# Kernel optimization log

Measured on AMD Instinct MI355X. Metric: run time of the kernel, lower is better.

The kernel has to match this reference:

```python
import jax, jax.numpy as jnp
import numpy as np

N_NODES = 100000
N_INCID = 2000000
N_HEDGES = 300000
IN_DIM = 92
H_DIM = 64
ATTR_DIM = 35
HOUT_DIM = 128
N_GRAPHS = 512
N_LAYERS = 3
MSG_DIM = 2 * H_DIM + ATTR_DIM  # 163, matches Linear(2*node_fea_dim+hedge_fea_dim, out_dim)


def _segment_mean(vals, ids, num_segments):
    s = jax.ops.segment_sum(vals, ids, num_segments=num_segments)
    c = jax.ops.segment_sum(jnp.ones((vals.shape[0],), vals.dtype), ids, num_segments=num_segments)
    return s / jnp.maximum(c, 1.0)[:, None]


def setup_inputs() -> dict:
    key = jax.random.key(0)
    ks = jax.random.split(key, 16)
    x = jax.random.normal(ks[0], (N_NODES, IN_DIM), jnp.float32)
    incid_nodes = jax.random.randint(ks[1], (N_INCID,), 0, N_NODES)
    incid_hedges = jax.random.randint(ks[2], (N_INCID,), 0, N_HEDGES)
    hedge_attr = jax.random.normal(ks[3], (N_HEDGES, ATTR_DIM), jnp.float32)
    batch = jnp.sort(jax.random.randint(ks[4], (N_NODES,), 0, N_GRAPHS))
    def lin(k, fi, fo):
        lim = 1.0 / np.sqrt(fi)
        kw, kb = jax.random.split(k)
        return (jax.random.uniform(kw, (fi, fo), jnp.float32, -lim, lim),
                jax.random.uniform(kb, (fo,), jnp.float32, -lim, lim))
    W_embed, b_embed = lin(ks[5], IN_DIM, H_DIM)
    Wf, bf = [], []
    Wc, bc = [], []
    for l in range(N_LAYERS):
        w, b = lin(jax.random.fold_in(ks[6], l), MSG_DIM, H_DIM)
        Wf.append(w); bf.append(b)
        w, b = lin(jax.random.fold_in(ks[7], l), MSG_DIM, H_DIM)
        Wc.append(w); bc.append(b)
    Wf = jnp.stack(Wf); bf = jnp.stack(bf)
    Wc = jnp.stack(Wc); bc = jnp.stack(bc)
    W_proj, b_proj = lin(ks[8], H_DIM, HOUT_DIM)
    W_out, b_out = lin(ks[9], HOUT_DIM, 1)
    return {"x": x, "incid_nodes": incid_nodes, "incid_hedges": incid_hedges,
            "hedge_attr": hedge_attr, "batch": batch,
            "W_embed": W_embed, "b_embed": b_embed,
            "Wf": Wf, "bf": bf, "Wc": Wc, "bc": bc,
            "W_proj": W_proj, "b_proj": b_proj, "W_out": W_out, "b_out": b_out}


def reference(x, incid_nodes, incid_hedges, hedge_attr, batch,
              W_embed, b_embed, Wf, bf, Wc, bc, W_proj, b_proj, W_out, b_out):
    h = x @ W_embed + b_embed  # [N, H_DIM] embed
    node_cnt = jax.ops.segment_sum(jnp.ones((N_INCID,), h.dtype), incid_nodes,
                                   num_segments=N_NODES)
    has_incid = (node_cnt > 0)[:, None]
    # mean of hedge_attr over hedges containing each node (constant across layers)
    node_a = _segment_mean(hedge_attr[incid_hedges], incid_nodes, N_NODES)
    for l in range(N_LAYERS):
        # per-hedge mean of member node features (the normalized node_hedge_adj @ x)
        hedge_mean = _segment_mean(h[incid_nodes], incid_hedges, N_HEDGES)  # [H, H_DIM]
        # per-node mean over incident hedges of the message components
        node_h = _segment_mean(hedge_mean[incid_hedges], incid_nodes, N_NODES)
        x_part = jnp.where(has_incid, h, 0.0)  # mean over incidences of constant x_i
        z = jnp.concatenate([x_part, node_h, node_a], axis=1)  # [N, MSG_DIM]
        z_f = z @ Wf[l] + bf[l]
        z_c = z @ Wc[l] + bc[l]
        h = jax.nn.softplus(jax.nn.sigmoid(z_f) * jax.nn.softplus(z_c) + h)
    pooled = _segment_mean(h, batch, N_GRAPHS)  # scatter-mean global pooling
    p = jax.nn.softplus(pooled @ W_proj + b_proj)
    return p @ W_out + b_out  # [N_GRAPHS, 1]
```

## Files before the change

### kernel.cpp

```cpp
#include <hip/hip_runtime.h>
#include <hip/hip_bf16.h>

#define N_NODES 100000
#define N_INCID 2000000
#define N_HEDGES 300000
#define IN_DIM 92
#define H_DIM 64
#define ATTR_DIM 35
#define ATTR_PAIRS 18
#define HOUT_DIM 128
#define N_GRAPHS 512
#define N_LAYERS 3
#define MSG_DIM 163
#define KPAIRS 96
#define ZLDS 100
#define EPAIRS 48
#define ELDS 50

#define IPB 8192
#define NBLK 245
#define ESHIFT 9
#define NB_E 586
#define NSHIFT 8
#define NB_N 391

typedef short bf16x8 __attribute__((ext_vector_type(8)));
typedef float f32x4 __attribute__((ext_vector_type(4)));

__device__ __forceinline__ float softplusf(float x) {
    return fmaxf(x, 0.f) + __logf(1.f + __expf(-fabsf(x)));
}
__device__ __forceinline__ float sigmoidf(float x) {
    return __builtin_amdgcn_rcpf(1.f + __expf(-x));
}
__device__ __forceinline__ float2 bf2_to_f2(unsigned v) {
    union { unsigned u; float f; } a, b;
    a.u = v << 16;
    b.u = v & 0xffff0000u;
    return make_float2(a.f, b.f);
}
__device__ __forceinline__ unsigned f2_to_bf2(float x, float y) {
    union { float f; unsigned u; } a, b;
    a.f = x; b.f = y;
    unsigned lo = (a.u + 0x7fffu + ((a.u >> 16) & 1u)) >> 16;
    unsigned hi = ((b.u + 0x7fffu + ((b.u >> 16) & 1u)) >> 16) << 16;
    return lo | hi;
}

__global__ void embpack_k(const float* __restrict__ W, unsigned* __restrict__ BtE) {
    int idx = blockIdx.x * 256 + threadIdx.x;
    if (idx >= 64 * EPAIRS) return;
    int c = idx / EPAIRS, p = idx - c * EPAIRS;
    int k0 = 2 * p, k1 = 2 * p + 1;
    float v0 = (k0 < IN_DIM) ? W[k0 * 64 + c] : 0.f;
    float v1 = (k1 < IN_DIM) ? W[k1 * 64 + c] : 0.f;
    BtE[idx] = f2_to_bf2(v0, v1);
}

__global__ void __launch_bounds__(256)
embed_mfma_k(const float* __restrict__ x, const unsigned* __restrict__ BtE,
             const float* __restrict__ be, const int* __restrict__ ncnt,
             float* __restrict__ h, unsigned* __restrict__ hb,
             unsigned* __restrict__ zb) {
    __shared__ unsigned zsu[64][ELDS];
    __shared__ unsigned btu[64][ELDS];
    int node0 = blockIdx.x * 64;
    int t = threadIdx.x;
    for (int idx = t; idx < 64 * EPAIRS; idx += 256) {
        int r = idx / EPAIRS, p = idx - r * EPAIRS;
        int node = node0 + r;
        unsigned pr = 0u;
        if (node < N_NODES && p < 46) {
            float2 f = *(const float2*)(x + (size_t)node * IN_DIM + 2 * p);
            pr = f2_to_bf2(f.x, f.y);
        }
        zsu[r][p] = pr;
    }
    for (int idx = t; idx < 64 * EPAIRS; idx += 256) {
        int c = idx / EPAIRS, p = idx - c * EPAIRS;
        btu[c][p] = BtE[idx];
    }
    __syncthreads();
    int w = t >> 6, lane = t & 63, row16 = lane & 15, kg = lane >> 4;
    f32x4 acc[4];
#pragma unroll
    for (int n = 0; n < 4; ++n) acc[n] = (f32x4){0.f, 0.f, 0.f, 0.f};
#pragma unroll
    for (int ks = 0; ks < 3; ++ks) {
        int pbase = ks * 16 + kg * 4;
        bf16x8 a = *(const bf16x8*)&zsu[w * 16 + row16][pbase];
#pragma unroll
        for (int n = 0; n < 4; ++n) {
            bf16x8 b = *(const bf16x8*)&btu[n * 16 + row16][pbase];
            acc[n] = __builtin_amdgcn_mfma_f32_16x16x32_bf16(a, b, acc[n], 0, 0, 0);
        }
    }
#pragma unroll
    for (int i = 0; i < 4; ++i) {
        int node = node0 + w * 16 + kg * 4 + i;
        if (node < N_NODES) {
            bool has = ncnt[node] > 0;
#pragma unroll
            for (int n = 0; n < 4; ++n) {
                int d = n * 16 + row16;
                float nv = acc[n][i] + be[d];
                h[node * 64 + d] = nv;
                float other = __shfl_xor(nv, 1);
                if ((d & 1) == 0) {
                    unsigned pr = f2_to_bf2(nv, other);
                    hb[node * 32 + (d >> 1)] = pr;
                    zb[(size_t)node * KPAIRS + (d >> 1)] = has ? pr : 0u;
                }
            }
        }
    }
}

__global__ void attrconv_k(const float* __restrict__ hattr, unsigned* __restrict__ hab) {
    int idx = blockIdx.x * 256 + threadIdx.x;
    if (idx >= N_HEDGES * ATTR_PAIRS) return;
    int e = idx / ATTR_PAIRS, p = idx - e * ATTR_PAIRS;
    int d0 = 2 * p, d1 = 2 * p + 1;
    float v0 = hattr[e * ATTR_DIM + d0];
    float v1 = (d1 < ATTR_DIM) ? hattr[e * ATTR_DIM + d1] : 0.f;
    hab[idx] = f2_to_bf2(v0, v1);
}

__global__ void btpack_k(const float* __restrict__ Wf, const float* __restrict__ Wc,
                         unsigned* __restrict__ Btb) {
    int idx = blockIdx.x * 256 + threadIdx.x;
    if (idx >= N_LAYERS * 128 * KPAIRS) return;
    int l = idx / (128 * KPAIRS);
    int rem = idx - l * 128 * KPAIRS;
    int c = rem / KPAIRS, p = rem - c * KPAIRS;
    int k0 = 2 * p, k1 = 2 * p + 1;
    const float* W = (c < 64) ? (Wf + (size_t)l * MSG_DIM * 64) : (Wc + (size_t)l * MSG_DIM * 64);
    int cc = c & 63;
    float v0 = (k0 < MSG_DIM) ? W[k0 * 64 + cc] : 0.f;
    float v1 = (k1 < MSG_DIM) ? W[k1 * 64 + cc] : 0.f;
    Btb[idx] = f2_to_bf2(v0, v1);
}

__global__ void sorthist_k(const int* __restrict__ key, int* __restrict__ hist,
                           int kshift, int NB) {
    __shared__ int cnt[640];
    int blk = blockIdx.x;
    for (int i = threadIdx.x; i < NB; i += 256) cnt[i] = 0;
    __syncthreads();
    int base = blk * IPB;
    int end = min(base + IPB, N_INCID);
    for (int i = base + threadIdx.x; i < end; i += 256)
        atomicAdd(&cnt[key[i] >> kshift], 1);
    __syncthreads();
    for (int i = threadIdx.x; i < NB; i += 256) hist[blk * NB + i] = cnt[i];
}

__global__ void scanR1_k(const int* __restrict__ in, int* __restrict__ out,
                         int* __restrict__ bsum, int n, int NB) {
    __shared__ int tmp[256];
    int gid = blockIdx.x * 256 + threadIdx.x;
    int v = 0;
    if (gid < n) {
        int bucket = gid / NBLK, blk = gid - bucket * NBLK;
        v = in[blk * NB + bucket];
    }
    tmp[threadIdx.x] = v;
    __syncthreads();
    for (int o = 1; o < 256; o <<= 1) {
        int t = (threadIdx.x >= o) ? tmp[threadIdx.x - o] : 0;
        __syncthreads();
        tmp[threadIdx.x] += t;
        __syncthreads();
    }
    if (gid < n) out[gid] = tmp[threadIdx.x] - v;
    if (threadIdx.x == 255) bsum[blockIdx.x] = tmp[255];
}

__global__ void scan2_k(int* __restrict__ bsum, int nb) {
    __shared__ int tmp[256];
    __shared__ int carry;
    if (threadIdx.x == 0) carry = 0;
    __syncthreads();
    for (int base = 0; base < nb; base += 256) {
        int gid = base + threadIdx.x;
        int v = (gid < nb) ? bsum[gid] : 0;
        tmp[threadIdx.x] = v;
        __syncthreads();
        for (int o = 1; o < 256; o <<= 1) {
            int t = (threadIdx.x >= o) ? tmp[threadIdx.x - o] : 0;
            __syncthreads();
            tmp[threadIdx.x] += t;
            __syncthreads();
        }
        if (gid < nb) bsum[gid] = tmp[threadIdx.x] - v + carry;
        __syncthreads();
        if (threadIdx.x == 0) carry += tmp[255];
        __syncthreads();
    }
}

__global__ void scan3_k(int* __restrict__ out, const int* __restrict__ bsum, int n) {
    int gid = blockIdx.x * 256 + threadIdx.x;
    if (gid < n) out[gid] += bsum[blockIdx.x];
}

__global__ void sortscat_k(const int* __restrict__ key, const int* __restrict__ val,
                           const int* __restrict__ soff, uint2* __restrict__ stage,
                           int kshift, int NB) {
    __shared__ int cur[640], bas[640];
    int blk = blockIdx.x;
    for (int i = threadIdx.x; i < NB; i += 256) {
        cur[i] = 0;
        bas[i] = soff[i * NBLK + blk];
    }
    __syncthreads();
    int base = blk * IPB;
    int end = min(base + IPB, N_INCID);
    for (int i = base + threadIdx.x; i < end; i += 256) {
        int k = key[i], b = k >> kshift;
        int d = bas[b] + atomicAdd(&cur[b], 1);
        stage[d] = make_uint2((unsigned)k, (unsigned)val[i]);
    }
}

__global__ void sortfine_k(const uint2* __restrict__ stage, const int* __restrict__ soff,
                           int* __restrict__ csr, int* __restrict__ koff,
                           float* __restrict__ krcp, int* __restrict__ kcnt,
                           int kshift, int NB, int NKEYS, int nlog) {
    __shared__ int cnt[512], off[512], cur[512];
    int b = blockIdx.x;
    int KPB = 1 << kshift;
    int kbase = b << kshift;
    int base = soff[b * NBLK];
    int end = (b == NB - 1) ? N_INCID : soff[(b + 1) * NBLK];
    for (int i = threadIdx.x; i < KPB; i += 256) cnt[i] = 0;
    __syncthreads();
    for (int i = base + threadIdx.x; i < end; i += 256)
        atomicAdd(&cnt[(int)stage[i].x - kbase], 1);
    __syncthreads();
    if (threadIdx.x == 0) {
        int run = 0;
        for (int k = 0; k < KPB; ++k) { off[k] = run; run += cnt[k]; }
    }
    __syncthreads();
    for (int k = threadIdx.x; k < KPB; k += 256) {
        int gk = kbase + k;
        if (gk < NKEYS) {
            koff[gk] = base + off[k];
            krcp[gk] = 1.0f / (float)max(cnt[k], 1);
            kcnt[gk] = cnt[k];
        }
        cur[k] = 0;
    }
    __syncthreads();
    for (int i = base + threadIdx.x; i < end; i += 256) {
        uint2 it = stage[i];
        int lk = (int)it.x - kbase;
        int pos = base + off[lk] + atomicAdd(&cur[lk], 1);
        csr[pos] = (int)it.y;
    }
}

__global__ void sentinel_k(int* __restrict__ eoff, int* __restrict__ noff) {
    if (threadIdx.x == 0) eoff[N_HEDGES] = N_INCID;
    if (threadIdx.x == 1) noff[N_NODES] = N_INCID;
}

__global__ void hmean_k(const int* __restrict__ eoff, const int* __restrict__ csr_en,
                        const uint2* __restrict__ hbv, const float* __restrict__ ercp,
                        uint2* __restrict__ hmv) {
    int idx = blockIdx.x * 256 + threadIdx.x;
    int e = idx >> 5, l = idx & 31;
    if (e >= N_HEDGES) return;
    int sub = l >> 4, q = l & 15;
    int s = eoff[e], t = eoff[e + 1];
    float a0 = 0.f, a1 = 0.f, a2 = 0.f, a3 = 0.f;
    for (int base = s; base < t; base += 32) {
        int cnt = min(32, t - base);
        int myidx = (base + l < t) ? csr_en[base + l] : 0;
        for (int j = 0; j < cnt; j += 16) {
            uint2 v[8];
#pragma unroll
            for (int w = 0; w < 8; ++w) {
                int mem = j + 2 * w + sub;
                int nq = __shfl(myidx, mem, 32);
                v[w] = (mem < cnt) ? hbv[nq * 16 + q] : make_uint2(0u, 0u);
            }
#pragma unroll
            for (int w = 0; w < 8; ++w) {
                float2 f0 = bf2_to_f2(v[w].x), f1 = bf2_to_f2(v[w].y);
                a0 += f0.x; a1 += f0.y; a2 += f1.x; a3 += f1.y;
            }
        }
    }
    a0 += __shfl_xor(a0, 16);
    a1 += __shfl_xor(a1, 16);
    a2 += __shfl_xor(a2, 16);
    a3 += __shfl_xor(a3, 16);
    if (sub == 0) {
        float rc = ercp[e];
        hmv[e * 16 + q] = make_uint2(f2_to_bf2(a0 * rc, a1 * rc), f2_to_bf2(a2 * rc, a3 * rc));
    }
}

__global__ void nodeh_k(const int* __restrict__ noff, const int* __restrict__ csr_ne,
                        const uint2* __restrict__ hmv, const float* __restrict__ nrcp,
                        uint2* __restrict__ zbv) {
    int idx = blockIdx.x * 256 + threadIdx.x;
    int n = idx >> 5, l = idx & 31;
    if (n >= N_NODES) return;
    int sub = l >> 4, q = l & 15;
    int s = noff[n], t = noff[n + 1];
    float a0 = 0.f, a1 = 0.f, a2 = 0.f, a3 = 0.f;
    for (int base = s; base < t; base += 32) {
        int cnt = min(32, t - base);
        int myidx = (base + l < t) ? csr_ne[base + l] : 0;
        for (int j = 0; j < cnt; j += 16) {
            uint2 v[8];
#pragma unroll
            for (int w = 0; w < 8; ++w) {
                int mem = j + 2 * w + sub;
                int eq = __shfl(myidx, mem, 32);
                v[w] = (mem < cnt) ? hmv[eq * 16 + q] : make_uint2(0u, 0u);
            }
#pragma unroll
            for (int w = 0; w < 8; ++w) {
                float2 f0 = bf2_to_f2(v[w].x), f1 = bf2_to_f2(v[w].y);
                a0 += f0.x; a1 += f0.y; a2 += f1.x; a3 += f1.y;
            }
        }
    }
    a0 += __shfl_xor(a0, 16);
    a1 += __shfl_xor(a1, 16);
    a2 += __shfl_xor(a2, 16);
    a3 += __shfl_xor(a3, 16);
    if (sub == 0) {
        float rc = nrcp[n];
        zbv[(size_t)n * (KPAIRS / 2) + 16 + q] =
            make_uint2(f2_to_bf2(a0 * rc, a1 * rc), f2_to_bf2(a2 * rc, a3 * rc));
    }
}

__global__ void nodea_k(const int* __restrict__ noff, const int* __restrict__ csr_ne,
                        const uint2* __restrict__ habv, const float* __restrict__ nrcp,
                        uint2* __restrict__ zbv) {
    int idx = blockIdx.x * 256 + threadIdx.x;
    int n = idx >> 5, l = idx & 31;
    if (n >= N_NODES) return;
    int sub = l >> 4, q = l & 15;
    bool act = (q < ATTR_PAIRS / 2);
    int s = noff[n], t = noff[n + 1];
    float a0 = 0.f, a1 = 0.f, a2 = 0.f, a3 = 0.f;
    for (int base = s; base < t; base += 32) {
        int cnt = min(32, t - base);
        int myidx = (base + l < t) ? csr_ne[base + l] : 0;
        for (int j = 0; j < cnt; j += 16) {
            uint2 v[8];
#pragma unroll
            for (int w = 0; w < 8; ++w) {
                int mem = j + 2 * w + sub;
                int eq = __shfl(myidx, mem, 32);
                v[w] = (act && mem < cnt) ? habv[eq * (ATTR_PAIRS / 2) + q] : make_uint2(0u, 0u);
            }
#pragma unroll
            for (int w = 0; w < 8; ++w) {
                float2 f0 = bf2_to_f2(v[w].x), f1 = bf2_to_f2(v[w].y);
                a0 += f0.x; a1 += f0.y; a2 += f1.x; a3 += f1.y;
            }
        }
    }
    a0 += __shfl_xor(a0, 16);
    a1 += __shfl_xor(a1, 16);
    a2 += __shfl_xor(a2, 16);
    a3 += __shfl_xor(a3, 16);
    if (sub == 0) {
        float rc = nrcp[n];
        uint2 pr = act ? make_uint2(f2_to_bf2(a0 * rc, a1 * rc), f2_to_bf2(a2 * rc, a3 * rc))
                       : make_uint2(0u, 0u);
        zbv[(size_t)n * (KPAIRS / 2) + 32 + q] = pr;
    }
}

__global__ void __launch_bounds__(256)
layer_mfma_k(const unsigned* __restrict__ Btl, const float* __restrict__ bfv,
             const float* __restrict__ bcv, const int* __restrict__ ncnt,
             unsigned* __restrict__ zb, float* __restrict__ h,
             unsigned* __restrict__ hb) {
    __shared__ unsigned zsu[64][ZLDS];
    int node0 = blockIdx.x * 64;
    int t = threadIdx.x;
    int w = t >> 6, lane = t & 63;
    int row16 = lane & 15, kg = lane >> 4;

    uint4 bregF[6], bregC[6];
    {
        const uint4* bv = (const uint4*)Btl;
        int colF = w * 16 + row16;
        int colC = colF + 64;
#pragma unroll
        for (int ks = 0; ks < 6; ++ks) {
            bregF[ks] = bv[colF * 24 + ks * 4 + kg];
            bregC[ks] = bv[colC * 24 + ks * 4 + kg];
        }
    }
    {
        const uint4* zv = (const uint4*)zb;
        for (int idx = t; idx < 64 * 24; idx += 256) {
            int r = idx / 24, p4 = idx - r * 24;
            int node = node0 + r;
            uint4 v = make_uint4(0u, 0u, 0u, 0u);
            if (node < N_NODES) v = zv[(size_t)node * 24 + p4];
            *(uint4*)&zsu[r][p4 * 4] = v;
        }
    }
    __syncthreads();

    f32x4 accF[4], accC[4];
#pragma unroll
    for (int n = 0; n < 4; ++n) {
        accF[n] = (f32x4){0.f, 0.f, 0.f, 0.f};
        accC[n] = (f32x4){0.f, 0.f, 0.f, 0.f};
    }

#pragma unroll
    for (int ks = 0; ks < 6; ++ks) {
        int pbase = ks * 16 + kg * 4;
        bf16x8 bF = *(const bf16x8*)&bregF[ks];
        bf16x8 bC = *(const bf16x8*)&bregC[ks];
#pragma unroll
        for (int rb = 0; rb < 4; ++rb) {
            bf16x8 a = *(const bf16x8*)&zsu[rb * 16 + row16][pbase];
            accF[rb] = __builtin_amdgcn_mfma_f32_16x16x32_bf16(a, bF, accF[rb], 0, 0, 0);
            accC[rb] = __builtin_amdgcn_mfma_f32_16x16x32_bf16(a, bC, accC[rb], 0, 0, 0);
        }
    }

    int d = w * 16 + row16;
    float bfd = bfv[d], bcd = bcv[d];
#pragma unroll
    for (int rb = 0; rb < 4; ++rb) {
#pragma unroll
        for (int i = 0; i < 4; ++i) {
            int node = node0 + rb * 16 + kg * 4 + i;
            if (node < N_NODES) {
                bool has = ncnt[node] > 0;
                float f = accF[rb][i] + bfd;
                float c = accC[rb][i] + bcd;
                float hv = h[node * 64 + d];
                float nv = softplusf(sigmoidf(f) * softplusf(c) + hv);
                h[node * 64 + d] = nv;
                float other = __shfl_xor(nv, 1);
                if ((d & 1) == 0) {
                    unsigned pr = f2_to_bf2(nv, other);
                    hb[node * 32 + (d >> 1)] = pr;
                    zb[(size_t)node * KPAIRS + (d >> 1)] = has ? pr : 0u;
                }
            }
        }
    }
}

__global__ void gstart_k(const int* __restrict__ batch, int* __restrict__ gstart) {
    int g = blockIdx.x * 256 + threadIdx.x;
    if (g > N_GRAPHS) return;
    int lo = 0, hi = N_NODES;
    while (lo < hi) {
        int mid = (lo + hi) >> 1;
        if (batch[mid] < g) lo = mid + 1; else hi = mid;
    }
    gstart[g] = lo;
}

__global__ void poolhead_k(const float* __restrict__ h, const int* __restrict__ gstart,
                           const float* __restrict__ Wp, const float* __restrict__ bp,
                           const float* __restrict__ Wo, const float* __restrict__ bo,
                           float* __restrict__ out) {
    __shared__ float partial[4][64];
    __shared__ float pm[64];
    __shared__ float pr[128];
    int g = blockIdx.x, t = threadIdx.x;
    int s = gstart[g], e = gstart[g + 1];
    int w = t >> 6, lane = t & 63;
    float acc = 0.f;
    for (int n = s + w; n < e; n += 4) acc += h[n * 64 + lane];
    partial[w][lane] = acc;
    __syncthreads();
    if (t < 64) {
        float c = fmaxf((float)(e - s), 1.0f);
        pm[t] = (partial[0][t] + partial[1][t] + partial[2][t] + partial[3][t]) / c;
    }
    __syncthreads();
    if (t < 128) {
        float a = bp[t];
#pragma unroll 4
        for (int k = 0; k < 64; ++k) a += pm[k] * Wp[k * HOUT_DIM + t];
        pr[t] = softplusf(a) * Wo[t];
    }
    __syncthreads();
    if (t < 64) {
        float v = pr[t] + pr[t + 64];
        for (int o = 32; o > 0; o >>= 1) v += __shfl_down(v, o);
        if (t == 0) out[g] = v + bo[0];
    }
}

extern "C" void kernel_launch(void* const* d_in, const int* in_sizes, int n_in,
                              void* d_out, int out_size, void* d_ws, size_t ws_size,
                              hipStream_t stream) {
    const float* x       = (const float*)d_in[0];
    const int*   inc_n   = (const int*)d_in[1];
    const int*   inc_e   = (const int*)d_in[2];
    const float* hattr   = (const float*)d_in[3];
    const int*   batch   = (const int*)d_in[4];
    const float* W_embed = (const float*)d_in[5];
    const float* b_embed = (const float*)d_in[6];
    const float* Wf      = (const float*)d_in[7];
    const float* bf      = (const float*)d_in[8];
    const float* Wc      = (const float*)d_in[9];
    const float* bc      = (const float*)d_in[10];
    const float* W_proj  = (const float*)d_in[11];
    const float* b_proj  = (const float*)d_in[12];
    const float* W_out   = (const float*)d_in[13];
    const float* b_out   = (const float*)d_in[14];
    float* out = (float*)d_out;

    char* ws = (char*)d_ws;
    size_t off = 0;
    auto alloc = [&](size_t bytes) {
        void* p = ws + off;
        off = (off + bytes + 255) & ~(size_t)255;
        return p;
    };
    float*    h      = (float*)alloc((size_t)N_NODES * 64 * 4);
    unsigned* hb     = (unsigned*)alloc((size_t)N_NODES * 32 * 4);
    unsigned* hmean  = (unsigned*)alloc((size_t)N_HEDGES * 32 * 4);
    unsigned* zb     = (unsigned*)alloc((size_t)N_NODES * KPAIRS * 4);
    unsigned* hab    = (unsigned*)alloc((size_t)N_HEDGES * ATTR_PAIRS * 4);
    unsigned* Btb    = (unsigned*)alloc((size_t)N_LAYERS * 128 * KPAIRS * 4);
    unsigned* BtE    = (unsigned*)alloc((size_t)64 * EPAIRS * 4);
    int*      ncnt   = (int*)alloc((size_t)N_NODES * 4);
    int*      ecnt   = (int*)alloc((size_t)N_HEDGES * 4);
    float*    nrcp   = (float*)alloc((size_t)N_NODES * 4);
    float*    ercp   = (float*)alloc((size_t)N_HEDGES * 4);
    int*      eoff   = (int*)alloc((size_t)(N_HEDGES + 1) * 4);
    int*      noff   = (int*)alloc((size_t)(N_NODES + 1) * 4);
    int*      csr_en = (int*)alloc((size_t)N_INCID * 4);
    int*      csr_ne = (int*)alloc((size_t)N_INCID * 4);
    int*      hist   = (int*)alloc((size_t)NB_E * NBLK * 4);
    int*      soff   = (int*)alloc((size_t)NB_E * NBLK * 4);
    int*      bsum   = (int*)alloc((size_t)2048 * 4);
    int*      gstart = (int*)alloc((size_t)(N_GRAPHS + 1) * 4);
    uint2*    stage  = (uint2*)hmean;

    {
        int nlog = NB_E * NBLK;
        int nsb = (nlog + 255) / 256;
        sorthist_k<<<NBLK, 256, 0, stream>>>(inc_e, hist, ESHIFT, NB_E);
        scanR1_k<<<nsb, 256, 0, stream>>>(hist, soff, bsum, nlog, NB_E);
        scan2_k<<<1, 256, 0, stream>>>(bsum, nsb);
        scan3_k<<<nsb, 256, 0, stream>>>(soff, bsum, nlog);
        sortscat_k<<<NBLK, 256, 0, stream>>>(inc_e, inc_n, soff, stage, ESHIFT, NB_E);
        sortfine_k<<<NB_E, 256, 0, stream>>>(stage, soff, csr_en, eoff, ercp, ecnt,
                                             ESHIFT, NB_E, N_HEDGES, nlog);
    }
    {
        int nlog = NB_N * NBLK;
        int nsb = (nlog + 255) / 256;
        sorthist_k<<<NBLK, 256, 0, stream>>>(inc_n, hist, NSHIFT, NB_N);
        scanR1_k<<<nsb, 256, 0, stream>>>(hist, soff, bsum, nlog, NB_N);
        scan2_k<<<1, 256, 0, stream>>>(bsum, nsb);
        scan3_k<<<nsb, 256, 0, stream>>>(soff, bsum, nlog);
        sortscat_k<<<NBLK, 256, 0, stream>>>(inc_n, inc_e, soff, stage, NSHIFT, NB_N);
        sortfine_k<<<NB_N, 256, 0, stream>>>(stage, soff, csr_ne, noff, nrcp, ncnt,
                                             NSHIFT, NB_N, N_NODES, nlog);
    }
    sentinel_k<<<1, 64, 0, stream>>>(eoff, noff);

    embpack_k<<<(64 * EPAIRS + 255) / 256, 256, 0, stream>>>(W_embed, BtE);
    embed_mfma_k<<<(N_NODES + 63) / 64, 256, 0, stream>>>(x, BtE, b_embed, ncnt, h, hb, zb);
    attrconv_k<<<(N_HEDGES * ATTR_PAIRS + 255) / 256, 256, 0, stream>>>(hattr, hab);
    btpack_k<<<(N_LAYERS * 128 * KPAIRS + 255) / 256, 256, 0, stream>>>(Wf, Wc, Btb);
    nodea_k<<<(N_NODES * 32) / 256, 256, 0, stream>>>(noff, csr_ne, (const uint2*)hab, nrcp,
                                                      (uint2*)zb);

    for (int l = 0; l < N_LAYERS; ++l) {
        hmean_k<<<(N_HEDGES * 32) / 256, 256, 0, stream>>>(eoff, csr_en, (const uint2*)hb, ercp,
                                                           (uint2*)hmean);
        nodeh_k<<<(N_NODES * 32) / 256, 256, 0, stream>>>(noff, csr_ne, (const uint2*)hmean, nrcp,
                                                          (uint2*)zb);
        layer_mfma_k<<<(N_NODES + 63) / 64, 256, 0, stream>>>(Btb + (size_t)l * 128 * KPAIRS,
                                                              bf + l * 64, bc + l * 64,
                                                              ncnt, zb, h, hb);
    }
    gstart_k<<<(N_GRAPHS + 1 + 255) / 256, 256, 0, stream>>>(batch, gstart);
    poolhead_k<<<N_GRAPHS, 256, 0, stream>>>(h, gstart, W_proj, b_proj, W_out, b_out, out);
}
```

Measured before the change: 639.2 us.

## Pack sort staging into 32-bit words, parallelize fine-sort scan, use packed f32x2 accumulation

```diff
diff --git a/kernel.cpp b/kernel.cpp
--- a/kernel.cpp
+++ b/kernel.cpp
@@ -23,9 +23,11 @@
 #define NB_E 586
 #define NSHIFT 8
 #define NB_N 391
+#define VALBITS 21
 
 typedef short bf16x8 __attribute__((ext_vector_type(8)));
 typedef float f32x4 __attribute__((ext_vector_type(4)));
+typedef float f32x2 __attribute__((ext_vector_type(2)));
 
 __device__ __forceinline__ float softplusf(float x) {
     return fmaxf(x, 0.f) + __logf(1.f + __expf(-fabsf(x)));
@@ -33,11 +35,11 @@
 __device__ __forceinline__ float sigmoidf(float x) {
     return __builtin_amdgcn_rcpf(1.f + __expf(-x));
 }
+__device__ __forceinline__ float u2f(unsigned u) {
+    union { unsigned u; float f; } x; x.u = u; return x.f;
+}
 __device__ __forceinline__ float2 bf2_to_f2(unsigned v) {
-    union { unsigned u; float f; } a, b;
-    a.u = v << 16;
-    b.u = v & 0xffff0000u;
-    return make_float2(a.f, b.f);
+    return make_float2(u2f(v << 16), u2f(v & 0xffff0000u));
 }
 __device__ __forceinline__ unsigned f2_to_bf2(float x, float y) {
     union { float f; unsigned u; } a, b;
@@ -205,7 +207,7 @@
 }
 
 __global__ void sortscat_k(const int* __restrict__ key, const int* __restrict__ val,
-                           const int* __restrict__ soff, uint2* __restrict__ stage,
+                           const int* __restrict__ soff, unsigned* __restrict__ stage,
                            int kshift, int NB) {
     __shared__ int cur[640], bas[640];
     int blk = blockIdx.x;
@@ -216,34 +218,48 @@
     __syncthreads();
     int base = blk * IPB;
     int end = min(base + IPB, N_INCID);
+    unsigned kmaskbits = (1u << kshift) - 1u;
     for (int i = base + threadIdx.x; i < end; i += 256) {
         int k = key[i], b = k >> kshift;
         int d = bas[b] + atomicAdd(&cur[b], 1);
-        stage[d] = make_uint2((unsigned)k, (unsigned)val[i]);
-    }
-}
-
-__global__ void sortfine_k(const uint2* __restrict__ stage, const int* __restrict__ soff,
+        stage[d] = (((unsigned)k & kmaskbits) << VALBITS) | (unsigned)val[i];
+    }
+}
+
+__global__ void sortfine_k(const unsigned* __restrict__ stage, const int* __restrict__ soff,
                            int* __restrict__ csr, int* __restrict__ koff,
                            float* __restrict__ krcp, int* __restrict__ kcnt,
-                           int kshift, int NB, int NKEYS, int nlog) {
+                           int kshift, int NB, int NKEYS) {
     __shared__ int cnt[512], off[512], cur[512];
+    __shared__ int ts[256];
     int b = blockIdx.x;
+    int tid = threadIdx.x;
     int KPB = 1 << kshift;
     int kbase = b << kshift;
     int base = soff[b * NBLK];
     int end = (b == NB - 1) ? N_INCID : soff[(b + 1) * NBLK];
-    for (int i = threadIdx.x; i < KPB; i += 256) cnt[i] = 0;
-    __syncthreads();
-    for (int i = base + threadIdx.x; i < end; i += 256)
-        atomicAdd(&cnt[(int)stage[i].x - kbase], 1);
-    __syncthreads();
-    if (threadIdx.x == 0) {
-        int run = 0;
-        for (int k = 0; k < KPB; ++k) { off[k] = run; run += cnt[k]; }
-    }
-    __syncthreads();
-    for (int k = threadIdx.x; k < KPB; k += 256) {
+    for (int i = tid; i < KPB; i += 256) cnt[i] = 0;
+    __syncthreads();
+    for (int i = base + tid; i < end; i += 256)
+        atomicAdd(&cnt[stage[i] >> VALBITS], 1);
+    __syncthreads();
+    int half = KPB >> 1;
+    int c0 = 0, c1 = 0;
+    if (tid < half) { c0 = cnt[2 * tid]; c1 = cnt[2 * tid + 1]; ts[tid] = c0 + c1; }
+    __syncthreads();
+    for (int o = 1; o < 256; o <<= 1) {
+        int v = (tid >= o && tid < half) ? ts[tid - o] : 0;
+        __syncthreads();
+        if (tid < half) ts[tid] += v;
+        __syncthreads();
+    }
+    if (tid < half) {
+        int ex = ts[tid] - (c0 + c1);
+        off[2 * tid] = ex;
+        off[2 * tid + 1] = ex + c0;
+    }
+    __syncthreads();
+    for (int k = tid; k < KPB; k += 256) {
         int gk = kbase + k;
         if (gk < NKEYS) {
             koff[gk] = base + off[k];
@@ -253,11 +269,11 @@
         cur[k] = 0;
     }
     __syncthreads();
-    for (int i = base + threadIdx.x; i < end; i += 256) {
-        uint2 it = stage[i];
-        int lk = (int)it.x - kbase;
+    for (int i = base + tid; i < end; i += 256) {
+        unsigned it = stage[i];
+        int lk = (int)(it >> VALBITS);
         int pos = base + off[lk] + atomicAdd(&cur[lk], 1);
-        csr[pos] = (int)it.y;
+        csr[pos] = (int)(it & ((1u << VALBITS) - 1u));
     }
 }
 
@@ -274,7 +290,7 @@
     if (e >= N_HEDGES) return;
     int sub = l >> 4, q = l & 15;
     int s = eoff[e], t = eoff[e + 1];
-    float a0 = 0.f, a1 = 0.f, a2 = 0.f, a3 = 0.f;
+    f32x2 A01 = {0.f, 0.f}, A23 = {0.f, 0.f};
     for (int base = s; base < t; base += 32) {
         int cnt = min(32, t - base);
         int myidx = (base + l < t) ? csr_en[base + l] : 0;
@@ -288,15 +304,15 @@
             }
 #pragma unroll
             for (int w = 0; w < 8; ++w) {
-                float2 f0 = bf2_to_f2(v[w].x), f1 = bf2_to_f2(v[w].y);
-                a0 += f0.x; a1 += f0.y; a2 += f1.x; a3 += f1.y;
-            }
-        }
-    }
-    a0 += __shfl_xor(a0, 16);
-    a1 += __shfl_xor(a1, 16);
-    a2 += __shfl_xor(a2, 16);
-    a3 += __shfl_xor(a3, 16);
+                A01 += (f32x2){u2f(v[w].x << 16), u2f(v[w].x)};
+                A23 += (f32x2){u2f(v[w].y << 16), u2f(v[w].y)};
+            }
+        }
+    }
+    float a0 = A01.x + __shfl_xor(A01.x, 16);
+    float a1 = A01.y + __shfl_xor(A01.y, 16);
+    float a2 = A23.x + __shfl_xor(A23.x, 16);
+    float a3 = A23.y + __shfl_xor(A23.y, 16);
     if (sub == 0) {
         float rc = ercp[e];
         hmv[e * 16 + q] = make_uint2(f2_to_bf2(a0 * rc, a1 * rc), f2_to_bf2(a2 * rc, a3 * rc));
@@ -311,7 +327,7 @@
     if (n >= N_NODES) return;
     int sub = l >> 4, q = l & 15;
     int s = noff[n], t = noff[n + 1];
-    float a0 = 0.f, a1 = 0.f, a2 = 0.f, a3 = 0.f;
+    f32x2 A01 = {0.f, 0.f}, A23 = {0.f, 0.f};
     for (int base = s; base < t; base += 32) {
         int cnt = min(32, t - base);
         int myidx = (base + l < t) ? csr_ne[base + l] : 0;
@@ -325,15 +341,15 @@
             }
 #pragma unroll
             for (int w = 0; w < 8; ++w) {
-                float2 f0 = bf2_to_f2(v[w].x), f1 = bf2_to_f2(v[w].y);
-                a0 += f0.x; a1 += f0.y; a2 += f1.x; a3 += f1.y;
-            }
-        }
-    }
-    a0 += __shfl_xor(a0, 16);
-    a1 += __shfl_xor(a1, 16);
-    a2 += __shfl_xor(a2, 16);
-    a3 += __shfl_xor(a3, 16);
+                A01 += (f32x2){u2f(v[w].x << 16), u2f(v[w].x)};
+                A23 += (f32x2){u2f(v[w].y << 16), u2f(v[w].y)};
+            }
+        }
+    }
+    float a0 = A01.x + __shfl_xor(A01.x, 16);
+    float a1 = A01.y + __shfl_xor(A01.y, 16);
+    float a2 = A23.x + __shfl_xor(A23.x, 16);
+    float a3 = A23.y + __shfl_xor(A23.y, 16);
     if (sub == 0) {
         float rc = nrcp[n];
         zbv[(size_t)n * (KPAIRS / 2) + 16 + q] =
@@ -350,7 +366,7 @@
     int sub = l >> 4, q = l & 15;
     bool act = (q < ATTR_PAIRS / 2);
     int s = noff[n], t = noff[n + 1];
-    float a0 = 0.f, a1 = 0.f, a2 = 0.f, a3 = 0.f;
+    f32x2 A01 = {0.f, 0.f}, A23 = {0.f, 0.f};
     for (int base = s; base < t; base += 32) {
         int cnt = min(32, t - base);
         int myidx = (base + l < t) ? csr_ne[base + l] : 0;
@@ -364,15 +380,15 @@
             }
 #pragma unroll
             for (int w = 0; w < 8; ++w) {
-                float2 f0 = bf2_to_f2(v[w].x), f1 = bf2_to_f2(v[w].y);
-                a0 += f0.x; a1 += f0.y; a2 += f1.x; a3 += f1.y;
-            }
-        }
-    }
-    a0 += __shfl_xor(a0, 16);
-    a1 += __shfl_xor(a1, 16);
-    a2 += __shfl_xor(a2, 16);
-    a3 += __shfl_xor(a3, 16);
+                A01 += (f32x2){u2f(v[w].x << 16), u2f(v[w].x)};
+                A23 += (f32x2){u2f(v[w].y << 16), u2f(v[w].y)};
+            }
+        }
+    }
+    float a0 = A01.x + __shfl_xor(A01.x, 16);
+    float a1 = A01.y + __shfl_xor(A01.y, 16);
+    float a2 = A23.x + __shfl_xor(A23.x, 16);
+    float a3 = A23.y + __shfl_xor(A23.y, 16);
     if (sub == 0) {
         float rc = nrcp[n];
         uint2 pr = act ? make_uint2(f2_to_bf2(a0 * rc, a1 * rc), f2_to_bf2(a2 * rc, a3 * rc))
@@ -550,7 +566,7 @@
     int*      soff   = (int*)alloc((size_t)NB_E * NBLK * 4);
     int*      bsum   = (int*)alloc((size_t)2048 * 4);
     int*      gstart = (int*)alloc((size_t)(N_GRAPHS + 1) * 4);
-    uint2*    stage  = (uint2*)hmean;
+    unsigned* stage  = (unsigned*)hmean;
 
     {
         int nlog = NB_E * NBLK;
@@ -561,7 +577,7 @@
         scan3_k<<<nsb, 256, 0, stream>>>(soff, bsum, nlog);
         sortscat_k<<<NBLK, 256, 0, stream>>>(inc_e, inc_n, soff, stage, ESHIFT, NB_E);
         sortfine_k<<<NB_E, 256, 0, stream>>>(stage, soff, csr_en, eoff, ercp, ecnt,
-                                             ESHIFT, NB_E, N_HEDGES, nlog);
+                                             ESHIFT, NB_E, N_HEDGES);
     }
     {
         int nlog = NB_N * NBLK;
@@ -572,7 +588,7 @@
         scan3_k<<<nsb, 256, 0, stream>>>(soff, bsum, nlog);
         sortscat_k<<<NBLK, 256, 0, stream>>>(inc_n, inc_e, soff, stage, NSHIFT, NB_N);
         sortfine_k<<<NB_N, 256, 0, stream>>>(stage, soff, csr_ne, noff, nrcp, ncnt,
-                                             NSHIFT, NB_N, N_NODES, nlog);
+                                             NSHIFT, NB_N, N_NODES);
     }
     sentinel_k<<<1, 64, 0, stream>>>(eoff, noff);
 
```

Result: slower. 718.9 us (+12.5%).
